# Kernel tuning notes

Hardware: AMD Instinct MI355X
Metric: run time of the kernel (lower is better)

The kernel has to match this reference:

```python
import jax, jax.numpy as jnp
import numpy as np

B, T, QD, KD, AD = 64, 2048, 512, 512, 512
SCALING = 1.0
NEG = -1e10


def setup_inputs() -> dict:
    key = jax.random.key(0)
    ks = jax.random.split(key, 10)
    s = 0.02
    return {
        "query": jax.random.normal(ks[0], (B, QD), jnp.float32),
        "keys": jax.random.normal(ks[1], (B, T, KD), jnp.float32),
        "value": jax.random.normal(ks[2], (B, T, KD), jnp.float32),
        "cover": jax.random.uniform(ks[3], (B, T), jnp.float32),
        "key_len": jax.random.randint(ks[4], (B,), T // 2, T + 1),
        "Wq": jax.random.normal(ks[5], (QD, AD), jnp.float32) * s,
        "bq": jnp.zeros((AD,), jnp.float32),
        "Wk": jax.random.normal(ks[6], (KD, AD), jnp.float32) * s,
        "Wc": jax.random.normal(ks[7], (1, AD), jnp.float32) * s,
        "Wo": jax.random.normal(ks[8], (AD, 1), jnp.float32) * s,
    }


def reference(query, keys, value, cover, key_len, Wq, bq, Wk, Wc, Wo):
    # projections
    q = query @ Wq + bq                      # [B, A]
    k = jnp.einsum("btd,da->bta", keys, Wk)  # [B, T, A]
    c = cover[..., None] * Wc[0]             # [B, T, A]  (Linear(1, A), no bias)
    # additive energy
    e = jnp.tanh(q[:, None, :] + k + c)      # [B, T, A]
    energy = jnp.einsum("bta,ao->bot", e, Wo)  # [B, 1, T]
    # mask padded positions (t >= key_len)
    mask = jnp.arange(T)[None, None, :] >= key_len[:, None, None]  # [B, 1, T]
    energy = jnp.where(mask, NEG, energy)
    attn = jax.nn.softmax(energy * SCALING, axis=2)  # [B, 1, T]
    context = jnp.einsum("bqt,btd->bqd", attn, value)[:, 0, :]  # [B, KD]
    return context, attn
```

## Files before the change

### kernel.cpp

```cpp
#include <hip/hip_runtime.h>
#include <hip/hip_bf16.h>

#define B_ 64
#define T_ 2048
#define D_ 512
#define A_ 512
#define BMT 128
#define BNT 256
#define NIT 4

typedef float f32x4_t __attribute__((ext_vector_type(4)));
typedef short bf16x8_t __attribute__((ext_vector_type(8)));

#define GLL16(g, l) __builtin_amdgcn_global_load_lds( \
    (const __attribute__((address_space(1))) void*)(g), \
    (__attribute__((address_space(3))) void*)(l), 16, 0, 0)

#define SBAR __builtin_amdgcn_s_barrier()
#define LGKM0 do { asm volatile("s_waitcnt lgkmcnt(0)" ::: "memory"); \
                   __builtin_amdgcn_sched_barrier(0); } while (0)
#define VMW(N) asm volatile("s_waitcnt vmcnt(" #N ")" ::: "memory")

__global__ void __launch_bounds__(256) qproj_kernel(
    const float* __restrict__ query, const float* __restrict__ Wq,
    const float* __restrict__ bq, float* __restrict__ qbuf) {
  __shared__ float qs[D_];
  const int b = blockIdx.x, tid = threadIdx.x;
  qs[tid] = query[b*D_ + tid];
  qs[tid+256] = query[b*D_ + tid + 256];
  __syncthreads();
  float a0 = bq[tid], a1 = bq[tid+256];
  for (int d = 0; d < D_; ++d) {
    const float qv = qs[d];
    a0 += qv * Wq[d*A_ + tid];
    a1 += qv * Wq[d*A_ + tid + 256];
  }
  qbuf[b*A_ + tid] = a0;
  qbuf[b*A_ + tid+256] = a1;
}

__global__ void __launch_bounds__(256) wkprep_kernel(
    const float* __restrict__ Wk, unsigned int* __restrict__ slab) {
  __shared__ float tile[64][65];
  const int kt = blockIdx.x >> 3;
  const int a0 = (blockIdx.x & 7) * 64;
  const int tid = threadIdx.x;
  #pragma unroll
  for (int p = 0; p < 16; ++p) {
    const int idx = p*256 + tid;
    const int k = idx >> 6, al = idx & 63;
    tile[k][al] = Wk[(kt*64 + k)*A_ + a0 + al];
  }
  __syncthreads();
  #pragma unroll
  for (int w = 0; w < 2; ++w) {
    const int idx = w*256 + tid;
    const int al = idx >> 3, c = idx & 7;
    const int a = a0 + al;
    const int n = a & 255;
    const int ctb = a >> 8;
    const int s = c ^ (n & 7);
    union { __hip_bfloat162 h[2]; uint2 u; } x, y;
    x.h[0] = __float22bfloat162_rn(make_float2(tile[c*8+0][al], tile[c*8+1][al]));
    x.h[1] = __float22bfloat162_rn(make_float2(tile[c*8+2][al], tile[c*8+3][al]));
    y.h[0] = __float22bfloat162_rn(make_float2(tile[c*8+4][al], tile[c*8+5][al]));
    y.h[1] = __float22bfloat162_rn(make_float2(tile[c*8+6][al], tile[c*8+7][al]));
    *(uint4*)(slab + ((kt*2 + ctb)*256 + n)*32 + s*4) =
        make_uint4(x.u.x, x.u.y, y.u.x, y.u.y);
  }
}

__global__ void __launch_bounds__(512, 2) energy_kernel(
    const float* __restrict__ keys, const float* __restrict__ cover,
    const int* __restrict__ key_len, const unsigned char* __restrict__ slabB,
    const float* __restrict__ qbuf, const float* __restrict__ Wc,
    const float* __restrict__ Wo, float* __restrict__ epart) {
  __shared__ __align__(16) unsigned char lds[106496];

  const int d = blockIdx.x;
  const int logical = (d & 7) * 256 + (d >> 3);
  const int ct = logical & 1;
  const int tt = (logical >> 1) & 15;
  const int b  = logical >> 5;
  const int t0 = tt * BMT;
  const int kl = key_len[b];
  if (t0 >= kl) return;

  const int tid = threadIdx.x;
  const int wid = tid >> 6, lane = tid & 63;
  const int lq = lane >> 4, lr = lane & 15;
  const int wm = wid >> 2, wn = wid & 3;
  const int sx = lr & 7;

  const int aRow = (wm*64 + lr)*128;
  const int aOff0 = ((lq    ) ^ sx) << 4;
  const int aOff1 = ((4 + lq) ^ sx) << 4;
  const int bRow = 32768 + (wn*64 + lr)*128;

  const int sr = tid >> 2, sq = tid & 3;
  const float* akey = keys + ((size_t)b*T_ + t0 + sr)*(size_t)D_ + sq*16;
  unsigned char* const awr = lds + sr*128;
  const int wofA = ((sq*2    ) ^ (sr & 7)) << 4;
  const int wofB = ((sq*2 + 1) ^ (sr & 7)) << 4;

  const unsigned char* bsl = slabB + (size_t)ct*32768 + tid*16;
  unsigned char* const bwr = lds + 32768 + tid*16;

  f32x4_t acc[4][4];
  #pragma unroll
  for (int i = 0; i < 4; ++i)
    #pragma unroll
    for (int j = 0; j < 4; ++j) acc[i][j] = 0.0f;

  bf16x8_t aF[4], bF[2];
  f32x4_t pA[4], qA[4];

#define AGLOAD(kt, ARR) { const float* p_ = akey + (kt)*64; \
    ARR[0] = *(const f32x4_t*)(p_);      ARR[1] = *(const f32x4_t*)(p_ + 4); \
    ARR[2] = *(const f32x4_t*)(p_ + 8);  ARR[3] = *(const f32x4_t*)(p_ + 12); }

#define APACK(buf, ARR) { union { __hip_bfloat162 h[2]; uint2 u; } x_, y_; \
    x_.h[0] = __float22bfloat162_rn(make_float2(ARR[0][0], ARR[0][1])); \
    x_.h[1] = __float22bfloat162_rn(make_float2(ARR[0][2], ARR[0][3])); \
    y_.h[0] = __float22bfloat162_rn(make_float2(ARR[1][0], ARR[1][1])); \
    y_.h[1] = __float22bfloat162_rn(make_float2(ARR[1][2], ARR[1][3])); \
    *(uint4*)(awr + (buf)*16384 + wofA) = make_uint4(x_.u.x, x_.u.y, y_.u.x, y_.u.y); \
    x_.h[0] = __float22bfloat162_rn(make_float2(ARR[2][0], ARR[2][1])); \
    x_.h[1] = __float22bfloat162_rn(make_float2(ARR[2][2], ARR[2][3])); \
    y_.h[0] = __float22bfloat162_rn(make_float2(ARR[3][0], ARR[3][1])); \
    y_.h[1] = __float22bfloat162_rn(make_float2(ARR[3][2], ARR[3][3])); \
    *(uint4*)(awr + (buf)*16384 + wofB) = make_uint4(x_.u.x, x_.u.y, y_.u.x, y_.u.y); }

#define BGLL4(kt, buf) { const unsigned char* g_ = bsl + (size_t)(kt)*65536; \
    unsigned char* l_ = bwr + (buf)*32768; \
    GLL16(g_, l_); GLL16(g_ + 8192, l_ + 8192); \
    GLL16(g_ + 16384, l_ + 16384); GLL16(g_ + 24576, l_ + 24576); }

#define DSRA(buf, kk) { const unsigned char* p_ = lds + (buf)*16384 + aRow + ((kk) ? aOff1 : aOff0); \
    aF[0] = *(const bf16x8_t*)(p_);        aF[1] = *(const bf16x8_t*)(p_ + 2048); \
    aF[2] = *(const bf16x8_t*)(p_ + 4096); aF[3] = *(const bf16x8_t*)(p_ + 6144); }

#define DSRB(buf, kk, nh) { const unsigned char* p_ = lds + (buf)*32768 + bRow + ((kk) ? aOff1 : aOff0) + (nh)*4096; \
    bF[0] = *(const bf16x8_t*)(p_); bF[1] = *(const bf16x8_t*)(p_ + 2048); }

#define MFMA8(nh) { _Pragma("unroll") for (int mf_ = 0; mf_ < 4; ++mf_) { \
    _Pragma("unroll") for (int c_ = 0; c_ < 2; ++c_) \
      acc[mf_][(nh)*2 + c_] = __builtin_amdgcn_mfma_f32_16x16x32_bf16( \
          aF[mf_], bF[c_], acc[mf_][(nh)*2 + c_], 0, 0, 0); } }

#define PH_TAIL(nh) SBAR; LGKM0; __builtin_amdgcn_s_setprio(1); MFMA8(nh); \
    __builtin_amdgcn_s_setprio(0); SBAR

  AGLOAD(0, pA); BGLL4(0, 0);
  AGLOAD(1, qA); BGLL4(1, 1);
  VMW(12); APACK(0, pA);
  VMW(4);  APACK(1, qA);
  VMW(0);
  LGKM0;
  SBAR;

  #pragma unroll
  for (int it = 0; it < NIT; ++it) {
    const int c1 = 2*it + 1, p0 = 2*it + 2, p1 = 2*it + 3;
    DSRA(0, 0); DSRB(0, 0, 0);
    if (it >= 1) { BGLL4(c1, 1); }
    PH_TAIL(0);
    DSRB(0, 0, 1);
    if (it <= 2) { AGLOAD(p0, pA); }
    PH_TAIL(1);
    DSRA(0, 1); DSRB(0, 1, 0);
    if (it >= 1) {
      if (it <= 2) { VMW(8); } else { VMW(4); }
      APACK(1, qA);
    }
    PH_TAIL(0);
    DSRB(0, 1, 1);
    if (it >= 1) { if (it <= 2) { VMW(4); } else { VMW(0); } }
    PH_TAIL(1);
    DSRA(1, 0); DSRB(1, 0, 0);
    if (it <= 2) { BGLL4(p0, 0); }
    PH_TAIL(0);
    DSRB(1, 0, 1);
    if (it <= 2) { VMW(4); APACK(0, pA); }
    PH_TAIL(1);
    DSRA(1, 1); DSRB(1, 1, 0);
    PH_TAIL(0);
    DSRB(1, 1, 1);
    if (it <= 2) { AGLOAD(p1, qA); VMW(4); }
    PH_TAIL(1);
  }

  float* red = (float*)(lds + 98304);
  const float* qn  = qbuf + b*A_ + ct*BNT + wn*64 + lr;
  const float* wcn = Wc + ct*BNT + wn*64 + lr;
  const float* won = Wo + ct*BNT + wn*64 + lr;
  const float* covp = cover + (size_t)b*T_ + t0 + wm*64 + lq*4;
  float cov[4][4];
  #pragma unroll
  for (int mf = 0; mf < 4; ++mf)
    #pragma unroll
    for (int j = 0; j < 4; ++j) cov[mf][j] = covp[mf*16 + j];

  float ep[4][4];
  #pragma unroll
  for (int mf = 0; mf < 4; ++mf)
    #pragma unroll
    for (int j = 0; j < 4; ++j) ep[mf][j] = 0.f;

  #pragma unroll
  for (int nf = 0; nf < 4; ++nf) {
    const float qv = qn[nf*16];
    const float wc = wcn[nf*16];
    const float wo = won[nf*16];
    #pragma unroll
    for (int mf = 0; mf < 4; ++mf)
      #pragma unroll
      for (int j = 0; j < 4; ++j) {
        float p = acc[mf][nf][j] + qv + cov[mf][j] * wc;
        p = fminf(fmaxf(p, -15.f), 15.f);
        const float t2 = __expf(2.f * p);
        ep[mf][j] += wo * ((t2 - 1.f) * __builtin_amdgcn_rcpf(t2 + 1.f));
      }
  }
  #pragma unroll
  for (int mf = 0; mf < 4; ++mf)
    #pragma unroll
    for (int j = 0; j < 4; ++j) {
      float v = ep[mf][j];
      v += __shfl_xor(v, 1); v += __shfl_xor(v, 2);
      v += __shfl_xor(v, 4); v += __shfl_xor(v, 8);
      ep[mf][j] = v;
    }
  if (lr == 0) {
    #pragma unroll
    for (int mf = 0; mf < 4; ++mf)
      #pragma unroll
      for (int j = 0; j < 4; ++j)
        red[wid*64 + mf*16 + lq*4 + j] = ep[mf][j];
  }
  __syncthreads();
  if (tid < BMT) {
    const int r = tid, wmr = r >> 6, ro = r & 63;
    epart[((size_t)ct*B_ + b)*T_ + t0 + r] =
        red[(wmr*4+0)*64 + ro] + red[(wmr*4+1)*64 + ro] +
        red[(wmr*4+2)*64 + ro] + red[(wmr*4+3)*64 + ro];
  }
}

__global__ void __launch_bounds__(1024) softmax_kernel(
    const float* __restrict__ epart, const int* __restrict__ key_len,
    float* __restrict__ attn) {
  __shared__ float sredM[16];
  __shared__ float sredS[16];
  const int b = blockIdx.x, tid = threadIdx.x;
  const int kl = key_len[b];
  float e0 = -3.0e38f, e1 = -3.0e38f;
  if (tid < kl)
    e0 = epart[(size_t)b*T_ + tid] + epart[((size_t)B_ + b)*T_ + tid];
  if (tid + 1024 < kl)
    e1 = epart[(size_t)b*T_ + tid+1024] + epart[((size_t)B_ + b)*T_ + tid+1024];
  float m = fmaxf(e0, e1);
  for (int s = 32; s; s >>= 1) m = fmaxf(m, __shfl_xor(m, s));
  if ((tid & 63) == 0) sredM[tid >> 6] = m;
  __syncthreads();
  float M = -3.0e38f;
  #pragma unroll
  for (int i = 0; i < 16; ++i) M = fmaxf(M, sredM[i]);
  const float p0 = (tid < kl) ? __expf(e0 - M) : 0.f;
  const float p1 = (tid + 1024 < kl) ? __expf(e1 - M) : 0.f;
  float s = p0 + p1;
  for (int k = 32; k; k >>= 1) s += __shfl_xor(s, k);
  if ((tid & 63) == 0) sredS[tid >> 6] = s;
  __syncthreads();
  float S = 0.f;
  #pragma unroll
  for (int i = 0; i < 16; ++i) S += sredS[i];
  const float inv = 1.f / S;
  attn[b*T_ + tid] = p0 * inv;
  attn[b*T_ + tid + 1024] = p1 * inv;
}

__global__ void __launch_bounds__(256) ctxpart_kernel(
    const float* __restrict__ value, const float* __restrict__ attn,
    const int* __restrict__ key_len, float* __restrict__ partial) {
  __shared__ float att_s[256];
  __shared__ float4 comb[128];
  const int b = blockIdx.y, ch = blockIdx.x;
  const int tid = threadIdx.x;
  const int c4 = tid & 127, half = tid >> 7;
  const int kl = key_len[b];
  const int tstart = ch * 256;
  const int tend = min(256, kl - tstart);
  float4 acc = make_float4(0.f, 0.f, 0.f, 0.f);
  if (tend > 0) {
    att_s[tid] = attn[b*T_ + tstart + tid];
    __syncthreads();
    const float4* vp = (const float4*)(value + ((size_t)b*T_ + tstart)*D_) + c4;
    for (int i = half; i < tend; i += 2) {
      const float w = att_s[i];
      const float4 v = vp[(size_t)i * 128];
      acc.x += w * v.x; acc.y += w * v.y; acc.z += w * v.z; acc.w += w * v.w;
    }
  }
  if (half == 1) comb[c4] = acc;
  __syncthreads();
  if (half == 0) {
    const float4 o = comb[c4];
    acc.x += o.x; acc.y += o.y; acc.z += o.z; acc.w += o.w;
    ((float4*)(partial + (size_t)(b*8 + ch)*D_))[c4] = acc;
  }
}

__global__ void __launch_bounds__(128) ctxsum_kernel(
    const float* __restrict__ partial, float* __restrict__ ctx) {
  const int b = blockIdx.x, tid = threadIdx.x;
  float4 s = make_float4(0.f, 0.f, 0.f, 0.f);
  #pragma unroll
  for (int c = 0; c < 8; ++c) {
    const float4 v = ((const float4*)(partial + (size_t)(b*8 + c)*D_))[tid];
    s.x += v.x; s.y += v.y; s.z += v.z; s.w += v.w;
  }
  ((float4*)(ctx + (size_t)b*D_))[tid] = s;
}

extern "C" void kernel_launch(void* const* d_in, const int* in_sizes, int n_in,
                              void* d_out, int out_size, void* d_ws, size_t ws_size,
                              hipStream_t stream) {
  const float* query  = (const float*)d_in[0];
  const float* keys   = (const float*)d_in[1];
  const float* value  = (const float*)d_in[2];
  const float* cover  = (const float*)d_in[3];
  const int*   key_len= (const int*)d_in[4];
  const float* Wq     = (const float*)d_in[5];
  const float* bq     = (const float*)d_in[6];
  const float* Wk     = (const float*)d_in[7];
  const float* Wc     = (const float*)d_in[8];
  const float* Wo     = (const float*)d_in[9];

  float* out = (float*)d_out;
  float* ctx_out  = out;
  float* attn_out = out + B_*A_;

  float* ws = (float*)d_ws;
  float* qbuf    = ws;
  float* epart   = ws + 32768;
  float* partial = ws + 32768 + 262144;
  unsigned int* slab = (unsigned int*)(ws + 32768 + 262144 + 262144);

  qproj_kernel<<<B_, 256, 0, stream>>>(query, Wq, bq, qbuf);
  wkprep_kernel<<<64, 256, 0, stream>>>(Wk, slab);
  energy_kernel<<<B_*(T_/BMT)*(A_/BNT), 512, 0, stream>>>(
      keys, cover, key_len, (const unsigned char*)slab, qbuf, Wc, Wo, epart);
  softmax_kernel<<<B_, 1024, 0, stream>>>(epart, key_len, attn_out);
  ctxpart_kernel<<<dim3(8, B_), 256, 0, stream>>>(value, attn_out, key_len, partial);
  ctxsum_kernel<<<B_, 128, 0, stream>>>(partial, ctx_out);
}
```

Measured before the change: 243.1 us.

## Halve energy GEMM N-tile to 128 with 256-thread blocks and finer context split

The energy kernel's attention-dim tile shrinks from 256 to 128 columns, with 4 waves per block instead of 8, smaller LDS, and a reworked Wk slab layout and A-load mapping. The softmax now sums four partial energies instead of two. The context reduction uses 16 chunks of 128 steps, and the q projection is spread over four column blocks. The aim is more blocks and better occupancy and parallelism, at the cost of reading each keys tile twice as often and writing and reading more partial buffers.

```diff
diff --git a/kernel.cpp b/kernel.cpp
--- a/kernel.cpp
+++ b/kernel.cpp
@@ -6,7 +6,7 @@
 #define D_ 512
 #define A_ 512
 #define BMT 128
-#define BNT 256
+#define BNT 128
 #define NIT 4
 
 typedef float f32x4_t __attribute__((ext_vector_type(4)));
@@ -21,22 +21,19 @@
                    __builtin_amdgcn_sched_barrier(0); } while (0)
 #define VMW(N) asm volatile("s_waitcnt vmcnt(" #N ")" ::: "memory")
 
-__global__ void __launch_bounds__(256) qproj_kernel(
+__global__ void __launch_bounds__(128) qproj_kernel(
     const float* __restrict__ query, const float* __restrict__ Wq,
     const float* __restrict__ bq, float* __restrict__ qbuf) {
   __shared__ float qs[D_];
   const int b = blockIdx.x, tid = threadIdx.x;
-  qs[tid] = query[b*D_ + tid];
-  qs[tid+256] = query[b*D_ + tid + 256];
-  __syncthreads();
-  float a0 = bq[tid], a1 = bq[tid+256];
-  for (int d = 0; d < D_; ++d) {
-    const float qv = qs[d];
-    a0 += qv * Wq[d*A_ + tid];
-    a1 += qv * Wq[d*A_ + tid + 256];
-  }
-  qbuf[b*A_ + tid] = a0;
-  qbuf[b*A_ + tid+256] = a1;
+  const int col = blockIdx.y * 128 + tid;
+  #pragma unroll
+  for (int p = 0; p < 4; ++p) qs[p*128 + tid] = query[b*D_ + p*128 + tid];
+  __syncthreads();
+  float a0 = bq[col];
+  #pragma unroll 8
+  for (int d = 0; d < D_; ++d) a0 += qs[d] * Wq[d*A_ + col];
+  qbuf[b*A_ + col] = a0;
 }
 
 __global__ void __launch_bounds__(256) wkprep_kernel(
@@ -57,31 +54,29 @@
     const int idx = w*256 + tid;
     const int al = idx >> 3, c = idx & 7;
     const int a = a0 + al;
-    const int n = a & 255;
-    const int ctb = a >> 8;
-    const int s = c ^ (n & 7);
+    const int s = c ^ (a & 7);
     union { __hip_bfloat162 h[2]; uint2 u; } x, y;
     x.h[0] = __float22bfloat162_rn(make_float2(tile[c*8+0][al], tile[c*8+1][al]));
     x.h[1] = __float22bfloat162_rn(make_float2(tile[c*8+2][al], tile[c*8+3][al]));
     y.h[0] = __float22bfloat162_rn(make_float2(tile[c*8+4][al], tile[c*8+5][al]));
     y.h[1] = __float22bfloat162_rn(make_float2(tile[c*8+6][al], tile[c*8+7][al]));
-    *(uint4*)(slab + ((kt*2 + ctb)*256 + n)*32 + s*4) =
+    *(uint4*)(slab + ((size_t)(kt*512 + a))*32 + s*4) =
         make_uint4(x.u.x, x.u.y, y.u.x, y.u.y);
   }
 }
 
-__global__ void __launch_bounds__(512, 2) energy_kernel(
+__global__ void __launch_bounds__(256, 2) energy_kernel(
     const float* __restrict__ keys, const float* __restrict__ cover,
     const int* __restrict__ key_len, const unsigned char* __restrict__ slabB,
     const float* __restrict__ qbuf, const float* __restrict__ Wc,
     const float* __restrict__ Wo, float* __restrict__ epart) {
-  __shared__ __align__(16) unsigned char lds[106496];
+  __shared__ __align__(16) unsigned char lds[66560];
 
   const int d = blockIdx.x;
-  const int logical = (d & 7) * 256 + (d >> 3);
-  const int ct = logical & 1;
-  const int tt = (logical >> 1) & 15;
-  const int b  = logical >> 5;
+  const int logical = (d & 7) * 512 + (d >> 3);
+  const int ct = logical & 3;
+  const int tt = (logical >> 2) & 15;
+  const int b  = logical >> 6;
   const int t0 = tt * BMT;
   const int kl = key_len[b];
   if (t0 >= kl) return;
@@ -89,21 +84,24 @@
   const int tid = threadIdx.x;
   const int wid = tid >> 6, lane = tid & 63;
   const int lq = lane >> 4, lr = lane & 15;
-  const int wm = wid >> 2, wn = wid & 3;
+  const int wm = wid >> 1, wn = wid & 1;
   const int sx = lr & 7;
 
   const int aRow = (wm*64 + lr)*128;
   const int aOff0 = ((lq    ) ^ sx) << 4;
   const int aOff1 = ((4 + lq) ^ sx) << 4;
-  const int bRow = 32768 + (wn*64 + lr)*128;
-
-  const int sr = tid >> 2, sq = tid & 3;
-  const float* akey = keys + ((size_t)b*T_ + t0 + sr)*(size_t)D_ + sq*16;
+  const int bRow = (wn*64 + lr)*128;
+
+  const int sr = tid >> 1, sh = tid & 1;
+  const float* akey = keys + ((size_t)b*T_ + t0 + sr)*(size_t)D_ + sh*32;
   unsigned char* const awr = lds + sr*128;
-  const int wofA = ((sq*2    ) ^ (sr & 7)) << 4;
-  const int wofB = ((sq*2 + 1) ^ (sr & 7)) << 4;
-
-  const unsigned char* bsl = slabB + (size_t)ct*32768 + tid*16;
+  const int srx = sr & 7;
+  const int wof0 = ((sh*4+0) ^ srx) << 4;
+  const int wof1 = ((sh*4+1) ^ srx) << 4;
+  const int wof2 = ((sh*4+2) ^ srx) << 4;
+  const int wof3 = ((sh*4+3) ^ srx) << 4;
+
+  const unsigned char* bsl = slabB + (size_t)ct*16384 + tid*16;
   unsigned char* const bwr = lds + 32768 + tid*16;
 
   f32x4_t acc[4][4];
@@ -113,34 +111,37 @@
     for (int j = 0; j < 4; ++j) acc[i][j] = 0.0f;
 
   bf16x8_t aF[4], bF[2];
-  f32x4_t pA[4], qA[4];
+  f32x4_t pA[8], qA[8];
 
 #define AGLOAD(kt, ARR) { const float* p_ = akey + (kt)*64; \
     ARR[0] = *(const f32x4_t*)(p_);      ARR[1] = *(const f32x4_t*)(p_ + 4); \
-    ARR[2] = *(const f32x4_t*)(p_ + 8);  ARR[3] = *(const f32x4_t*)(p_ + 12); }
-
-#define APACK(buf, ARR) { union { __hip_bfloat162 h[2]; uint2 u; } x_, y_; \
-    x_.h[0] = __float22bfloat162_rn(make_float2(ARR[0][0], ARR[0][1])); \
-    x_.h[1] = __float22bfloat162_rn(make_float2(ARR[0][2], ARR[0][3])); \
-    y_.h[0] = __float22bfloat162_rn(make_float2(ARR[1][0], ARR[1][1])); \
-    y_.h[1] = __float22bfloat162_rn(make_float2(ARR[1][2], ARR[1][3])); \
-    *(uint4*)(awr + (buf)*16384 + wofA) = make_uint4(x_.u.x, x_.u.y, y_.u.x, y_.u.y); \
-    x_.h[0] = __float22bfloat162_rn(make_float2(ARR[2][0], ARR[2][1])); \
-    x_.h[1] = __float22bfloat162_rn(make_float2(ARR[2][2], ARR[2][3])); \
-    y_.h[0] = __float22bfloat162_rn(make_float2(ARR[3][0], ARR[3][1])); \
-    y_.h[1] = __float22bfloat162_rn(make_float2(ARR[3][2], ARR[3][3])); \
-    *(uint4*)(awr + (buf)*16384 + wofB) = make_uint4(x_.u.x, x_.u.y, y_.u.x, y_.u.y); }
+    ARR[2] = *(const f32x4_t*)(p_ + 8);  ARR[3] = *(const f32x4_t*)(p_ + 12); \
+    ARR[4] = *(const f32x4_t*)(p_ + 16); ARR[5] = *(const f32x4_t*)(p_ + 20); \
+    ARR[6] = *(const f32x4_t*)(p_ + 24); ARR[7] = *(const f32x4_t*)(p_ + 28); }
+
+#define PK16(dst, va, vb) { union { __hip_bfloat162 h[2]; uint2 u; } x_, y_; \
+    x_.h[0] = __float22bfloat162_rn(make_float2(va[0], va[1])); \
+    x_.h[1] = __float22bfloat162_rn(make_float2(va[2], va[3])); \
+    y_.h[0] = __float22bfloat162_rn(make_float2(vb[0], vb[1])); \
+    y_.h[1] = __float22bfloat162_rn(make_float2(vb[2], vb[3])); \
+    *(uint4*)(dst) = make_uint4(x_.u.x, x_.u.y, y_.u.x, y_.u.y); }
+
+#define APACK(buf, ARR) { \
+    PK16(awr + (buf)*16384 + wof0, ARR[0], ARR[1]); \
+    PK16(awr + (buf)*16384 + wof1, ARR[2], ARR[3]); \
+    PK16(awr + (buf)*16384 + wof2, ARR[4], ARR[5]); \
+    PK16(awr + (buf)*16384 + wof3, ARR[6], ARR[7]); }
 
 #define BGLL4(kt, buf) { const unsigned char* g_ = bsl + (size_t)(kt)*65536; \
-    unsigned char* l_ = bwr + (buf)*32768; \
-    GLL16(g_, l_); GLL16(g_ + 8192, l_ + 8192); \
-    GLL16(g_ + 16384, l_ + 16384); GLL16(g_ + 24576, l_ + 24576); }
+    unsigned char* l_ = bwr + (buf)*16384; \
+    GLL16(g_, l_); GLL16(g_ + 4096, l_ + 4096); \
+    GLL16(g_ + 8192, l_ + 8192); GLL16(g_ + 12288, l_ + 12288); }
 
 #define DSRA(buf, kk) { const unsigned char* p_ = lds + (buf)*16384 + aRow + ((kk) ? aOff1 : aOff0); \
     aF[0] = *(const bf16x8_t*)(p_);        aF[1] = *(const bf16x8_t*)(p_ + 2048); \
     aF[2] = *(const bf16x8_t*)(p_ + 4096); aF[3] = *(const bf16x8_t*)(p_ + 6144); }
 
-#define DSRB(buf, kk, nh) { const unsigned char* p_ = lds + (buf)*32768 + bRow + ((kk) ? aOff1 : aOff0) + (nh)*4096; \
+#define DSRB(buf, kk, nh) { const unsigned char* p_ = lds + 32768 + (buf)*16384 + bRow + ((kk) ? aOff1 : aOff0) + (nh)*4096; \
     bF[0] = *(const bf16x8_t*)(p_); bF[1] = *(const bf16x8_t*)(p_ + 2048); }
 
 #define MFMA8(nh) { _Pragma("unroll") for (int mf_ = 0; mf_ < 4; ++mf_) { \
@@ -153,7 +154,7 @@
 
   AGLOAD(0, pA); BGLL4(0, 0);
   AGLOAD(1, qA); BGLL4(1, 1);
-  VMW(12); APACK(0, pA);
+  VMW(16); APACK(0, pA);
   VMW(4);  APACK(1, qA);
   VMW(0);
   LGKM0;
@@ -170,12 +171,12 @@
     PH_TAIL(1);
     DSRA(0, 1); DSRB(0, 1, 0);
     if (it >= 1) {
-      if (it <= 2) { VMW(8); } else { VMW(4); }
+      if (it <= 2) { VMW(12); } else { VMW(4); }
       APACK(1, qA);
     }
     PH_TAIL(0);
     DSRB(0, 1, 1);
-    if (it >= 1) { if (it <= 2) { VMW(4); } else { VMW(0); } }
+    if (it >= 1) { if (it <= 2) { VMW(8); } else { VMW(0); } }
     PH_TAIL(1);
     DSRA(1, 0); DSRB(1, 0, 0);
     if (it <= 2) { BGLL4(p0, 0); }
@@ -186,11 +187,11 @@
     DSRA(1, 1); DSRB(1, 1, 0);
     PH_TAIL(0);
     DSRB(1, 1, 1);
-    if (it <= 2) { AGLOAD(p1, qA); VMW(4); }
+    if (it <= 2) { AGLOAD(p1, qA); VMW(8); }
     PH_TAIL(1);
   }
 
-  float* red = (float*)(lds + 98304);
+  float* red = (float*)(lds + 65536);
   const float* qn  = qbuf + b*A_ + ct*BNT + wn*64 + lr;
   const float* wcn = Wc + ct*BNT + wn*64 + lr;
   const float* won = Wo + ct*BNT + wn*64 + lr;
@@ -241,9 +242,7 @@
   __syncthreads();
   if (tid < BMT) {
     const int r = tid, wmr = r >> 6, ro = r & 63;
-    epart[((size_t)ct*B_ + b)*T_ + t0 + r] =
-        red[(wmr*4+0)*64 + ro] + red[(wmr*4+1)*64 + ro] +
-        red[(wmr*4+2)*64 + ro] + red[(wmr*4+3)*64 + ro];
+    epart[((size_t)ct*B_ + b)*T_ + t0 + r] = red[wmr*128 + ro] + red[wmr*128 + 64 + ro];
   }
 }
 
@@ -256,9 +255,11 @@
   const int kl = key_len[b];
   float e0 = -3.0e38f, e1 = -3.0e38f;
   if (tid < kl)
-    e0 = epart[(size_t)b*T_ + tid] + epart[((size_t)B_ + b)*T_ + tid];
+    e0 = epart[(size_t)b*T_ + tid] + epart[((size_t)B_ + b)*T_ + tid]
+       + epart[((size_t)2*B_ + b)*T_ + tid] + epart[((size_t)3*B_ + b)*T_ + tid];
   if (tid + 1024 < kl)
-    e1 = epart[(size_t)b*T_ + tid+1024] + epart[((size_t)B_ + b)*T_ + tid+1024];
+    e1 = epart[(size_t)b*T_ + tid+1024] + epart[((size_t)B_ + b)*T_ + tid+1024]
+       + epart[((size_t)2*B_ + b)*T_ + tid+1024] + epart[((size_t)3*B_ + b)*T_ + tid+1024];
   float m = fmaxf(e0, e1);
   for (int s = 32; s; s >>= 1) m = fmaxf(m, __shfl_xor(m, s));
   if ((tid & 63) == 0) sredM[tid >> 6] = m;
@@ -283,17 +284,17 @@
 __global__ void __launch_bounds__(256) ctxpart_kernel(
     const float* __restrict__ value, const float* __restrict__ attn,
     const int* __restrict__ key_len, float* __restrict__ partial) {
-  __shared__ float att_s[256];
+  __shared__ float att_s[128];
   __shared__ float4 comb[128];
   const int b = blockIdx.y, ch = blockIdx.x;
   const int tid = threadIdx.x;
   const int c4 = tid & 127, half = tid >> 7;
   const int kl = key_len[b];
-  const int tstart = ch * 256;
-  const int tend = min(256, kl - tstart);
+  const int tstart = ch * 128;
+  const int tend = min(128, kl - tstart);
   float4 acc = make_float4(0.f, 0.f, 0.f, 0.f);
   if (tend > 0) {
-    att_s[tid] = attn[b*T_ + tstart + tid];
+    if (tid < 128) att_s[tid] = attn[b*T_ + tstart + tid];
     __syncthreads();
     const float4* vp = (const float4*)(value + ((size_t)b*T_ + tstart)*D_) + c4;
     for (int i = half; i < tend; i += 2) {
@@ -307,7 +308,7 @@
   if (half == 0) {
     const float4 o = comb[c4];
     acc.x += o.x; acc.y += o.y; acc.z += o.z; acc.w += o.w;
-    ((float4*)(partial + (size_t)(b*8 + ch)*D_))[c4] = acc;
+    ((float4*)(partial + (size_t)(b*16 + ch)*D_))[c4] = acc;
   }
 }
 
@@ -316,8 +317,8 @@
   const int b = blockIdx.x, tid = threadIdx.x;
   float4 s = make_float4(0.f, 0.f, 0.f, 0.f);
   #pragma unroll
-  for (int c = 0; c < 8; ++c) {
-    const float4 v = ((const float4*)(partial + (size_t)(b*8 + c)*D_))[tid];
+  for (int c = 0; c < 16; ++c) {
+    const float4 v = ((const float4*)(partial + (size_t)(b*16 + c)*D_))[tid];
     s.x += v.x; s.y += v.y; s.z += v.z; s.w += v.w;
   }
   ((float4*)(ctx + (size_t)b*D_))[tid] = s;
@@ -344,14 +345,14 @@
   float* ws = (float*)d_ws;
   float* qbuf    = ws;
   float* epart   = ws + 32768;
-  float* partial = ws + 32768 + 262144;
-  unsigned int* slab = (unsigned int*)(ws + 32768 + 262144 + 262144);
-
-  qproj_kernel<<<B_, 256, 0, stream>>>(query, Wq, bq, qbuf);
+  float* partial = ws + 32768 + 524288;
+  unsigned int* slab = (unsigned int*)(ws + 32768 + 524288 + 524288);
+
+  qproj_kernel<<<dim3(B_, 4), 128, 0, stream>>>(query, Wq, bq, qbuf);
   wkprep_kernel<<<64, 256, 0, stream>>>(Wk, slab);
-  energy_kernel<<<B_*(T_/BMT)*(A_/BNT), 512, 0, stream>>>(
+  energy_kernel<<<B_*(T_/BMT)*(A_/BNT), 256, 0, stream>>>(
       keys, cover, key_len, (const unsigned char*)slab, qbuf, Wc, Wo, epart);
   softmax_kernel<<<B_, 1024, 0, stream>>>(epart, key_len, attn_out);
-  ctxpart_kernel<<<dim3(8, B_), 256, 0, stream>>>(value, attn_out, key_len, partial);
+  ctxpart_kernel<<<dim3(16, B_), 256, 0, stream>>>(value, attn_out, key_len, partial);
   ctxsum_kernel<<<B_, 128, 0, stream>>>(partial, ctx_out);
 }
```

Measured after the change: 260.0 us. 7.0% more time.
